# Kernel optimization log

Hardware: AMD Instinct MI355X
Metric: run time of the kernel (lower is better)

Reference implementation:

```python
import jax, jax.numpy as jnp
import numpy as np

EPS = 1e-5

def _bn(x, gamma, beta, mean, var):
    # eval-mode BatchNorm2d
    inv = gamma / jnp.sqrt(var + EPS)
    return x * inv[None, :, None, None] + (beta - mean * inv)[None, :, None, None]

def _conv(x, w):
    # Conv2d kernel 3x3, padding=(1,0), no bias; width already circularly padded
    return jax.lax.conv_general_dilated(x, w, (1, 1), [(1, 1), (0, 0)],
                                        dimension_numbers=('NCHW', 'OIHW', 'NCHW'))

def _circ_pad_w(x):
    # F.pad(x, (1,1,0,0), mode='circular')
    return jnp.pad(x, ((0, 0), (0, 0), (0, 0), (1, 1)), mode='wrap')

def _forward(flow_matrix, polar_fea, range_fea,
             fusion_w, fusion_gamma, fusion_beta, fusion_mean, fusion_var,
             attn_w, attn_gamma, attn_beta, attn_mean, attn_var):
    N, C, Hr, Wr = range_fea.shape
    _, _, H, W = polar_fea.shape
    _, h, w, K, _ = flow_matrix.shape
    # nearest-resize flow grid to (H, W) (identity when h==H, w==W)
    ri = jnp.arange(H) * h // H
    ci = jnp.arange(W) * w // W
    flow = flow_matrix[:, ri][:, :, ci]                       # [N,H,W,K,2]
    # torch.flip(dims=[-1]) then pad z=0: grid x=flow[...,1], y=flow[...,0], z=0.
    # Din=1 and z=0 with align_corners=False => iz=0 exactly -> pure 2D bilinear.
    gx = flow[..., 1]
    gy = flow[..., 0]
    ix = ((gx + 1.0) * Wr - 1.0) * 0.5                        # [N,H,W,K]
    iy = ((gy + 1.0) * Hr - 1.0) * 0.5
    feat_flat = range_fea.reshape(N, C, Hr * Wr)

    def gather(yi, xi):
        # yi, xi: [N,H,W] int32; zeros padding outside
        valid = (yi >= 0) & (yi < Hr) & (xi >= 0) & (xi < Wr)
        lin = jnp.clip(yi, 0, Hr - 1) * Wr + jnp.clip(xi, 0, Wr - 1)
        v = jax.vmap(lambda f, l: jnp.take(f, l.reshape(-1), axis=1))(feat_flat, lin)
        v = v.reshape(N, C, H, W)
        return v * valid[:, None].astype(v.dtype)

    def step(carry, grid_k):
        ixk, iyk = grid_k                                     # [N,H,W]
        x0 = jnp.floor(ixk); y0 = jnp.floor(iyk)
        wx1 = ixk - x0;      wy1 = iyk - y0
        x0i = x0.astype(jnp.int32); y0i = y0.astype(jnp.int32)
        val = (((1 - wy1) * (1 - wx1))[:, None] * gather(y0i,     x0i)
             + ((1 - wy1) * wx1)[:, None]       * gather(y0i,     x0i + 1)
             + (wy1 * (1 - wx1))[:, None]       * gather(y0i + 1, x0i)
             + (wy1 * wx1)[:, None]             * gather(y0i + 1, x0i + 1))
        return jnp.maximum(carry, val), None

    init = jnp.full((N, C, H, W), -jnp.inf, range_fea.dtype)
    grids = (jnp.moveaxis(ix, -1, 0), jnp.moveaxis(iy, -1, 0))  # [K,N,H,W]
    flow_fea, _ = jax.lax.scan(step, init, grids)               # max over K samples

    fea = jnp.concatenate([polar_fea, flow_fea], axis=1)        # [N,2C,H,W]
    res = _conv(_circ_pad_w(fea), fusion_w)
    res = jax.nn.relu(_bn(res, fusion_gamma, fusion_beta, fusion_mean, fusion_var))
    att = _conv(_circ_pad_w(res), attn_w)
    att = jax.nn.softmax(_bn(att, attn_gamma, attn_beta, attn_mean, attn_var), axis=1)
    return polar_fea + res * att


def setup_inputs() -> dict:
    key = jax.random.key(0)
    ks = jax.random.split(key, 6)
    N, C, H, W, K, Hr, Wr = 1, 64, 480, 360, 32, 64, 2048
    flow_matrix = jax.random.uniform(ks[0], (N, H, W, K, 2), jnp.float32, -1.0, 1.0)
    polar_fea = jax.random.normal(ks[1], (N, C, H, W), jnp.float32)
    range_fea = jax.random.normal(ks[2], (N, C, Hr, Wr), jnp.float32)
    fusion_w = jax.random.normal(ks[3], (C, 2 * C, 3, 3), jnp.float32) * 0.02
    attn_w = jax.random.normal(ks[4], (C, C, 3, 3), jnp.float32) * 0.02
    ones = jnp.ones((C,), jnp.float32)
    zeros = jnp.zeros((C,), jnp.float32)
    return {
        'flow_matrix': flow_matrix, 'polar_fea': polar_fea, 'range_fea': range_fea,
        'fusion_w': fusion_w, 'fusion_gamma': ones, 'fusion_beta': zeros,
        'fusion_mean': zeros, 'fusion_var': ones,
        'attn_w': attn_w, 'attn_gamma': ones, 'attn_beta': zeros,
        'attn_mean': zeros, 'attn_var': ones,
    }


def reference(flow_matrix, polar_fea, range_fea,
              fusion_w, fusion_gamma, fusion_beta, fusion_mean, fusion_var,
              attn_w, attn_gamma, attn_beta, attn_mean, attn_var):
    return _forward(flow_matrix, polar_fea, range_fea,
                    fusion_w, fusion_gamma, fusion_beta, fusion_mean, fusion_var,
                    attn_w, attn_gamma, attn_beta, attn_mean, attn_var)
```

## Files before the change

### kernel.cpp

```cpp
#include <hip/hip_runtime.h>
#include <math.h>

#define CCH 64
#define HH 480
#define WW 360
#define KK 32
#define HR 64
#define WR 2048
#define NPIX (HH*WW)
#define RFNPIX (HR*WR)
#define ZOFF 16777216u
#define NEGOFF 16777344u

typedef __attribute__((ext_vector_type(8))) short short8;
typedef __attribute__((ext_vector_type(4))) float f32x4;
typedef __attribute__((ext_vector_type(4))) int  int4_;

__device__ __forceinline__ ushort f2bf(float f) {
    uint u = __float_as_uint(f);
    return (ushort)((u + 0x7fffu + ((u >> 16) & 1u)) >> 16);
}

__global__ __launch_bounds__(256) void k_wprep(const float* __restrict__ fw,
                                               const float* __restrict__ aw,
                                               ushort* __restrict__ wA1,
                                               ushort* __restrict__ wA2) {
    int t = blockIdx.x * 256 + threadIdx.x;
    if (t < 73728) {
        int j = t & 7, ln = (t >> 3) & 63, Mf = (t >> 9) & 3, rem = t >> 11;
        int tap = rem % 9, c = rem / 9;
        int o = Mf * 16 + (ln & 15);
        int ci = c * 32 + ((ln >> 4) & 3) * 8 + j;
        wA1[t] = f2bf(fw[(o * 128 + ci) * 9 + tap]);
    } else if (t < 73728 + 36864) {
        int i = t - 73728;
        int j = i & 7, ln = (i >> 3) & 63, Mf = (i >> 9) & 3, rem = i >> 11;
        int tap = rem % 9, c = rem / 9;
        int o = Mf * 16 + (ln & 15);
        int ci = c * 32 + ((ln >> 4) & 3) * 8 + j;
        wA2[i] = f2bf(aw[(o * 64 + ci) * 9 + tap]);
    }
}

__global__ __launch_bounds__(256) void k_tr(const float* __restrict__ src,
                                            ushort* __restrict__ dst,
                                            int npix, int rowShorts) {
    __shared__ float lds[64][65];
    int t = threadIdx.x;
    int pix0 = blockIdx.x * 64;
    int lx = t & 63, ty = t >> 6;
    #pragma unroll
    for (int cc = 0; cc < 64; cc += 4) {
        int c = cc + ty;
        lds[c][lx] = src[(size_t)c * npix + pix0 + lx];
    }
    __syncthreads();
    int cp = t & 31, po = t >> 5;
    #pragma unroll
    for (int pl = po; pl < 64; pl += 8) {
        uint u = (uint)f2bf(lds[2 * cp][pl]) | ((uint)f2bf(lds[2 * cp + 1][pl]) << 16);
        *(uint*)(dst + (size_t)(pix0 + pl) * rowShorts + cp * 2) = u;
    }
}

__global__ void k_zero(uint* __restrict__ rft32) {
    int t = threadIdx.x;
    if (t < 32)       rft32[(ZOFF >> 2) + t] = 0;
    else if (t < 64)  rft32[(NEGOFF >> 2) + (t - 32)] = 0xFF7FFF7Fu;
}

__global__ __launch_bounds__(256) void k_sample(const float* __restrict__ flow,
                                                const char* __restrict__ rftb,
                                                ushort* __restrict__ xin,
                                                int sel, int mergePrev) {
    __shared__ __align__(16) uint pbuf[4][2][33][8];
    int tid = threadIdx.x;
    int ln = tid & 63;
    int wid = tid >> 6;
    int half = ln >> 5;
    int gwave = blockIdx.x * 4 + wid;

    int k = ln & 31;
    int pix = gwave * 2 + half;
    const float* fp = flow + (size_t)pix * 64 + 2 * k;
    float gy = __builtin_nontemporal_load(fp);
    float gx = __builtin_nontemporal_load(fp + 1);
    float ix = fmaf(gx, 1024.f, 1023.5f);
    float iy = fmaf(gy, 32.f, 31.5f);
    float xf = floorf(ix), yf = floorf(iy);
    float wx = ix - xf, wy = iy - yf;
    int x0 = (int)xf, y0 = (int)yf;
    bool xv0 = (unsigned)x0 < (unsigned)WR;
    bool xv1 = (unsigned)(x0 + 1) < (unsigned)WR;
    bool yv0 = (unsigned)y0 < (unsigned)HR;
    bool yv1 = (unsigned)(y0 + 1) < (unsigned)HR;
    int xc0 = x0 < 0 ? 0 : x0;
    int xc1 = x0 + 1 > WR - 1 ? WR - 1 : x0 + 1;
    int yc0 = y0 < 0 ? 0 : y0;
    int yc1 = y0 + 1 > HR - 1 ? HR - 1 : y0 + 1;
    uint o00 = (xv0 && yv0) ? (uint)(((yc0 << 11) + xc0) << 7) : ZOFF;
    uint o01 = (xv1 && yv0) ? (uint)(((yc0 << 11) + xc1) << 7) : ZOFF;
    uint o10 = (xv0 && yv1) ? (uint)(((yc1 << 11) + xc0) << 7) : ZOFF;
    uint o11 = (xv1 && yv1) ? (uint)(((yc1 << 11) + xc1) << 7) : ZOFF;
    float w00 = (1.f - wy) * (1.f - wx);
    float w01 = (1.f - wy) * wx;
    float w10 = wy * (1.f - wx);
    float w11 = wy * wx;

    bool isIn = ((yc0 >> 5) == sel);
    unsigned long long hm = half ? 0xFFFFFFFF00000000ull : 0x00000000FFFFFFFFull;
    unsigned long long lower = (1ull << ln) - 1ull;
    unsigned long long balIn = __ballot(isIn);
    int cntIn = __popcll(balIn & hm);
    int rankIn = __popcll(balIn & hm & lower);
    int rankOut = __popcll(~balIn & hm & lower);
    int pos = isIn ? rankIn : (cntIn + rankOut);
    *(int4_*)&pbuf[wid][half][pos][0] =
        (int4_){(int)o00, __float_as_int(w00), (int)o01, __float_as_int(w01)};
    *(int4_*)&pbuf[wid][half][pos][4] =
        (int4_){(int)o10, __float_as_int(w10), (int)o11, __float_as_int(w11)};
    if ((ln & 31) == 0) {
        *(int4_*)&pbuf[wid][half][32][0] =
            (int4_){(int)NEGOFF, __float_as_int(1.0f), (int)ZOFF, 0};
        *(int4_*)&pbuf[wid][half][32][4] = (int4_){(int)ZOFF, 0, (int)ZOFF, 0};
    }
    __syncthreads();

    uint laneByte = (uint)((ln & 31) * 4);
    const uint* pb = &pbuf[wid][half][0][0];
    float mLo = -3.0e38f, mHi = -3.0e38f;
    int cA = __builtin_amdgcn_readlane(cntIn, 0);
    int cB = __builtin_amdgcn_readlane(cntIn, 32);
    int trip = cA > cB ? cA : cB;

    for (int i = 0; i < trip; i++) {
        int idx = (i < cntIn) ? i : 32;
        const uint* e = pb + idx * 8;
        uint2 e0 = *(const uint2*)(e + 0);
        uint2 e1 = *(const uint2*)(e + 2);
        uint2 e2 = *(const uint2*)(e + 4);
        uint2 e3 = *(const uint2*)(e + 6);
        uint d0 = *(const uint*)(rftb + (e0.x + laneByte));
        uint d1 = *(const uint*)(rftb + (e1.x + laneByte));
        uint d2 = *(const uint*)(rftb + (e2.x + laneByte));
        uint d3 = *(const uint*)(rftb + (e3.x + laneByte));
        float W0 = __uint_as_float(e0.y);
        float W1 = __uint_as_float(e1.y);
        float W2 = __uint_as_float(e2.y);
        float W3 = __uint_as_float(e3.y);

        float vlo = W0 * __uint_as_float(d0 << 16);
        vlo = fmaf(W1, __uint_as_float(d1 << 16), vlo);
        vlo = fmaf(W2, __uint_as_float(d2 << 16), vlo);
        vlo = fmaf(W3, __uint_as_float(d3 << 16), vlo);
        float vhi = W0 * __uint_as_float(d0 & 0xffff0000u);
        vhi = fmaf(W1, __uint_as_float(d1 & 0xffff0000u), vhi);
        vhi = fmaf(W2, __uint_as_float(d2 & 0xffff0000u), vhi);
        vhi = fmaf(W3, __uint_as_float(d3 & 0xffff0000u), vhi);
        mLo = fmaxf(mLo, vlo);
        mHi = fmaxf(mHi, vhi);
    }

    uint* xp = (uint*)((char*)xin + (size_t)pix * 256 + 128 + (ln & 31) * 4);
    if (mergePrev) {
        uint cur = __builtin_nontemporal_load(xp);
        mLo = fmaxf(mLo, __uint_as_float(cur << 16));
        mHi = fmaxf(mHi, __uint_as_float(cur & 0xffff0000u));
    }
    uint outw;
    asm("v_cvt_pk_bf16_f32 %0, %1, %2" : "=v"(outw) : "v"(mLo), "v"(mHi));
    __builtin_nontemporal_store(outw, xp);
}

__global__ __launch_bounds__(256) void k_mconv1(const ushort* __restrict__ xin,
                                                const ushort* __restrict__ wA,
                                                const float* __restrict__ g,
                                                const float* __restrict__ b,
                                                const float* __restrict__ mn,
                                                const float* __restrict__ vr,
                                                ushort* __restrict__ res_bf) {
    __shared__ __align__(16) ushort xt[3][194][32];
    int tid = threadIdx.x;
    int h = blockIdx.x >> 1, w0 = (blockIdx.x & 1) * 180;
    int wid = tid >> 6, ln = tid & 63;
    f32x4 acc[4][3];
    #pragma unroll
    for (int m = 0; m < 4; m++)
        #pragma unroll
        for (int nf = 0; nf < 3; nf++) acc[m][nf] = (f32x4){0.f, 0.f, 0.f, 0.f};

    for (int c = 0; c < 4; c++) {
        __syncthreads();
        for (int i = tid; i < 2184; i += 256) {
            int q = i & 3, s = i >> 2;
            int r = s / 182, pw = s - r * 182;
            int gh = h + r - 1;
            int gw = w0 + pw - 1;
            if (gw < 0) gw += WW;
            if (gw >= WW) gw -= WW;
            int4_ val = {0, 0, 0, 0};
            if ((unsigned)gh < (unsigned)HH)
                val = *(const int4_*)(xin + ((size_t)(gh * WW + gw) * 128 + c * 32 + q * 8));
            *(int4_*)&xt[r][pw][(q ^ (pw & 3)) * 8] = val;
        }
        __syncthreads();
        #pragma unroll
        for (int tap = 0; tap < 9; tap++) {
            int dh = tap / 3, dw = tap % 3;
            short8 aF[4];
            #pragma unroll
            for (int m = 0; m < 4; m++)
                aF[m] = *(const short8*)(wA + (size_t)(((c * 9 + tap) * 4 + m) * 64 + ln) * 8);
            short8 bF[3];
            #pragma unroll
            for (int nf = 0; nf < 3; nf++) {
                int pw = wid * 48 + nf * 16 + (ln & 15) + dw;
                bF[nf] = *(const short8*)&xt[dh][pw][((((ln >> 4) & 3)) ^ (pw & 3)) * 8];
            }
            #pragma unroll
            for (int m = 0; m < 4; m++)
                #pragma unroll
                for (int nf = 0; nf < 3; nf++)
                    acc[m][nf] = __builtin_amdgcn_mfma_f32_16x16x32_bf16(aF[m], bF[nf], acc[m][nf], 0, 0, 0);
        }
    }
    #pragma unroll
    for (int m = 0; m < 4; m++) {
        int ob = m * 16 + ((ln >> 4) & 3) * 4;
        float sc0 = g[ob]     * rsqrtf(vr[ob]     + 1e-5f);
        float sc1 = g[ob + 1] * rsqrtf(vr[ob + 1] + 1e-5f);
        float sc2 = g[ob + 2] * rsqrtf(vr[ob + 2] + 1e-5f);
        float sc3 = g[ob + 3] * rsqrtf(vr[ob + 3] + 1e-5f);
        float bi0 = b[ob]     - mn[ob]     * sc0;
        float bi1 = b[ob + 1] - mn[ob + 1] * sc1;
        float bi2 = b[ob + 2] - mn[ob + 2] * sc2;
        float bi3 = b[ob + 3] - mn[ob + 3] * sc3;
        #pragma unroll
        for (int nf = 0; nf < 3; nf++) {
            int n = wid * 48 + nf * 16 + (ln & 15);
            if (n < 180) {
                int P = h * WW + w0 + n;
                float v0 = fmaxf(fmaf(acc[m][nf][0], sc0, bi0), 0.f);
                float v1 = fmaxf(fmaf(acc[m][nf][1], sc1, bi1), 0.f);
                float v2 = fmaxf(fmaf(acc[m][nf][2], sc2, bi2), 0.f);
                float v3 = fmaxf(fmaf(acc[m][nf][3], sc3, bi3), 0.f);
                uint lo, hi;
                asm("v_cvt_pk_bf16_f32 %0, %1, %2" : "=v"(lo) : "v"(v0), "v"(v1));
                asm("v_cvt_pk_bf16_f32 %0, %1, %2" : "=v"(hi) : "v"(v2), "v"(v3));
                uint2 pk; pk.x = lo; pk.y = hi;
                *(uint2*)(res_bf + (size_t)P * 64 + ob) = pk;
            }
        }
    }
}

__global__ __launch_bounds__(256) void k_mconv2(const ushort* __restrict__ res_bf,
                                                const float* __restrict__ polar,
                                                const ushort* __restrict__ wA,
                                                const float* __restrict__ g,
                                                const float* __restrict__ b,
                                                const float* __restrict__ mn,
                                                const float* __restrict__ vr,
                                                float* __restrict__ out) {
    __shared__ __align__(16) ushort xt[3][194][32];
    int tid = threadIdx.x;
    int h = blockIdx.x >> 1, w0 = (blockIdx.x & 1) * 180;
    int wid = tid >> 6, ln = tid & 63;
    f32x4 acc[4][3];
    #pragma unroll
    for (int m = 0; m < 4; m++)
        #pragma unroll
        for (int nf = 0; nf < 3; nf++) acc[m][nf] = (f32x4){0.f, 0.f, 0.f, 0.f};

    for (int c = 0; c < 2; c++) {
        __syncthreads();
        for (int i = tid; i < 2184; i += 256) {
            int q = i & 3, s = i >> 2;
            int r = s / 182, pw = s - r * 182;
            int gh = h + r - 1;
            int gw = w0 + pw - 1;
            if (gw < 0) gw += WW;
            if (gw >= WW) gw -= WW;
            int4_ val = {0, 0, 0, 0};
            if ((unsigned)gh < (unsigned)HH)
                val = *(const int4_*)(res_bf + ((size_t)(gh * WW + gw) * 64 + c * 32 + q * 8));
            *(int4_*)&xt[r][pw][(q ^ (pw & 3)) * 8] = val;
        }
        __syncthreads();
        #pragma unroll
        for (int tap = 0; tap < 9; tap++) {
            int dh = tap / 3, dw = tap % 3;
            short8 aF[4];
            #pragma unroll
            for (int m = 0; m < 4; m++)
                aF[m] = *(const short8*)(wA + (size_t)(((c * 9 + tap) * 4 + m) * 64 + ln) * 8);
            short8 bF[3];
            #pragma unroll
            for (int nf = 0; nf < 3; nf++) {
                int pw = wid * 48 + nf * 16 + (ln & 15) + dw;
                bF[nf] = *(const short8*)&xt[dh][pw][((((ln >> 4) & 3)) ^ (pw & 3)) * 8];
            }
            #pragma unroll
            for (int m = 0; m < 4; m++)
                #pragma unroll
                for (int nf = 0; nf < 3; nf++)
                    acc[m][nf] = __builtin_amdgcn_mfma_f32_16x16x32_bf16(aF[m], bF[nf], acc[m][nf], 0, 0, 0);
        }
    }
    #pragma unroll
    for (int m = 0; m < 4; m++) {
        #pragma unroll
        for (int reg = 0; reg < 4; reg++) {
            int o = m * 16 + ((ln >> 4) & 3) * 4 + reg;
            float sc = g[o] * rsqrtf(vr[o] + 1e-5f);
            float bi = b[o] - mn[o] * sc;
            #pragma unroll
            for (int nf = 0; nf < 3; nf++)
                acc[m][nf][reg] = fmaf(acc[m][nf][reg], sc, bi);
        }
    }
    #pragma unroll
    for (int nf = 0; nf < 3; nf++) {
        float mx = -3.0e38f;
        #pragma unroll
        for (int m = 0; m < 4; m++)
            #pragma unroll
            for (int reg = 0; reg < 4; reg++) mx = fmaxf(mx, acc[m][nf][reg]);
        mx = fmaxf(mx, __shfl_xor(mx, 16));
        mx = fmaxf(mx, __shfl_xor(mx, 32));
        float s = 0.f;
        #pragma unroll
        for (int m = 0; m < 4; m++)
            #pragma unroll
            for (int reg = 0; reg < 4; reg++) {
                float e = __expf(acc[m][nf][reg] - mx);
                acc[m][nf][reg] = e;
                s += e;
            }
        s += __shfl_xor(s, 16);
        s += __shfl_xor(s, 32);
        float rinv = 1.f / s;
        int n = wid * 48 + nf * 16 + (ln & 15);
        if (n < 180) {
            int P = h * WW + w0 + n;
            #pragma unroll
            for (int m = 0; m < 4; m++)
                #pragma unroll
                for (int reg = 0; reg < 4; reg++) {
                    int o = m * 16 + ((ln >> 4) & 3) * 4 + reg;
                    float att = acc[m][nf][reg] * rinv;
                    float rv = __uint_as_float((uint)res_bf[(size_t)P * 64 + o] << 16);
                    out[(size_t)o * NPIX + P] =
                        fmaf(rv, att, polar[(size_t)o * NPIX + P]);
                }
        }
    }
}

extern "C" void kernel_launch(void* const* d_in, const int* in_sizes, int n_in,
                              void* d_out, int out_size, void* d_ws, size_t ws_size,
                              hipStream_t stream) {
    const float* flow  = (const float*)d_in[0];
    const float* polar = (const float*)d_in[1];
    const float* rf    = (const float*)d_in[2];
    const float* fw    = (const float*)d_in[3];
    const float* fg    = (const float*)d_in[4];
    const float* fb    = (const float*)d_in[5];
    const float* fm    = (const float*)d_in[6];
    const float* fv    = (const float*)d_in[7];
    const float* aw    = (const float*)d_in[8];
    const float* ag    = (const float*)d_in[9];
    const float* ab    = (const float*)d_in[10];
    const float* am    = (const float*)d_in[11];
    const float* av    = (const float*)d_in[12];
    float* out = (float*)d_out;

    char* wsb = (char*)d_ws;
    ushort* xin    = (ushort*)wsb;
    ushort* rft    = (ushort*)(wsb + 44236800);
    ushort* res_bf = (ushort*)(wsb + 61014272);
    ushort* wA1    = (ushort*)(wsb + 83132672);
    ushort* wA2    = wA1 + 73728;

    k_wprep<<<432, 256, 0, stream>>>(fw, aw, wA1, wA2);
    k_tr<<<NPIX / 64, 256, 0, stream>>>(polar, xin, NPIX, 128);
    k_tr<<<RFNPIX / 64, 256, 0, stream>>>(rf, rft, RFNPIX, 64);
    k_zero<<<1, 64, 0, stream>>>((uint*)rft);
    k_sample<<<NPIX / 8, 256, 0, stream>>>(flow, (const char*)rft, xin, 0, 0);
    k_sample<<<NPIX / 8, 256, 0, stream>>>(flow, (const char*)rft, xin, 1, 1);
    k_mconv1<<<960, 256, 0, stream>>>(xin, wA1, fg, fb, fm, fv, res_bf);
    k_mconv2<<<960, 256, 0, stream>>>(res_bf, polar, wA2, ag, ab, am, av, out);
}
```

Measured before the change: 364.5 us.

## Load conv B-fragments directly from global memory instead of LDS staging

Both 3x3 conv MFMA kernels drop the shared-memory tile and its two barriers per channel chunk. Each lane now reads its bf16 input fragments straight from global memory using precomputed circular-wrapped column offsets, and skips rows that fall outside the image. This removes the LDS write/read round trip and the synchronisation, relying on L1/L2 to serve the neighbouring taps that reuse the same data. The cost is more global load instructions and exposed latency per MFMA group, with no LDS reuse across waves.

Measured after the change: 410.5 us. 12.6% more time.

```diff
diff --git a/kernel.cpp b/kernel.cpp
--- a/kernel.cpp
+++ b/kernel.cpp
@@ -179,54 +179,57 @@
                                                 const float* __restrict__ mn,
                                                 const float* __restrict__ vr,
                                                 ushort* __restrict__ res_bf) {
-    __shared__ __align__(16) ushort xt[3][194][32];
     int tid = threadIdx.x;
     int h = blockIdx.x >> 1, w0 = (blockIdx.x & 1) * 180;
     int wid = tid >> 6, ln = tid & 63;
-    f32x4 acc[4][3];
-    #pragma unroll
-    for (int m = 0; m < 4; m++)
-        #pragma unroll
-        for (int nf = 0; nf < 3; nf++) acc[m][nf] = (f32x4){0.f, 0.f, 0.f, 0.f};
-
-    for (int c = 0; c < 4; c++) {
-        __syncthreads();
-        for (int i = tid; i < 2184; i += 256) {
-            int q = i & 3, s = i >> 2;
-            int r = s / 182, pw = s - r * 182;
-            int gh = h + r - 1;
-            int gw = w0 + pw - 1;
+    int kq = (ln >> 4) & 3;
+    int nl = ln & 15;
+
+    int poff[3][3];
+    #pragma unroll
+    for (int dw = 0; dw < 3; dw++)
+        #pragma unroll
+        for (int nf = 0; nf < 3; nf++) {
+            int gw = w0 + wid * 48 + nf * 16 + nl + dw - 1;
             if (gw < 0) gw += WW;
             if (gw >= WW) gw -= WW;
-            int4_ val = {0, 0, 0, 0};
-            if ((unsigned)gh < (unsigned)HH)
-                val = *(const int4_*)(xin + ((size_t)(gh * WW + gw) * 128 + c * 32 + q * 8));
-            *(int4_*)&xt[r][pw][(q ^ (pw & 3)) * 8] = val;
-        }
-        __syncthreads();
-        #pragma unroll
-        for (int tap = 0; tap < 9; tap++) {
-            int dh = tap / 3, dw = tap % 3;
-            short8 aF[4];
-            #pragma unroll
-            for (int m = 0; m < 4; m++)
-                aF[m] = *(const short8*)(wA + (size_t)(((c * 9 + tap) * 4 + m) * 64 + ln) * 8);
-            short8 bF[3];
-            #pragma unroll
-            for (int nf = 0; nf < 3; nf++) {
-                int pw = wid * 48 + nf * 16 + (ln & 15) + dw;
-                bF[nf] = *(const short8*)&xt[dh][pw][((((ln >> 4) & 3)) ^ (pw & 3)) * 8];
+            poff[dw][nf] = gw * 128;
+        }
+
+    f32x4 acc[4][3];
+    #pragma unroll
+    for (int m = 0; m < 4; m++)
+        #pragma unroll
+        for (int nf = 0; nf < 3; nf++) acc[m][nf] = (f32x4){0.f, 0.f, 0.f, 0.f};
+
+    for (int c = 0; c < 4; c++) {
+        #pragma unroll
+        for (int dh = 0; dh < 3; dh++) {
+            int gh = h + dh - 1;
+            if ((unsigned)gh >= (unsigned)HH) continue;
+            const ushort* rowp = xin + (size_t)gh * (WW * 128) + c * 32 + kq * 8;
+            #pragma unroll
+            for (int dw = 0; dw < 3; dw++) {
+                int tap = dh * 3 + dw;
+                short8 aF[4];
+                #pragma unroll
+                for (int m = 0; m < 4; m++)
+                    aF[m] = *(const short8*)(wA + (size_t)(((c * 9 + tap) * 4 + m) * 64 + ln) * 8);
+                short8 bF[3];
+                #pragma unroll
+                for (int nf = 0; nf < 3; nf++)
+                    bF[nf] = *(const short8*)(rowp + poff[dw][nf]);
+                #pragma unroll
+                for (int m = 0; m < 4; m++)
+                    #pragma unroll
+                    for (int nf = 0; nf < 3; nf++)
+                        acc[m][nf] = __builtin_amdgcn_mfma_f32_16x16x32_bf16(aF[m], bF[nf], acc[m][nf], 0, 0, 0);
             }
-            #pragma unroll
-            for (int m = 0; m < 4; m++)
-                #pragma unroll
-                for (int nf = 0; nf < 3; nf++)
-                    acc[m][nf] = __builtin_amdgcn_mfma_f32_16x16x32_bf16(aF[m], bF[nf], acc[m][nf], 0, 0, 0);
         }
     }
     #pragma unroll
     for (int m = 0; m < 4; m++) {
-        int ob = m * 16 + ((ln >> 4) & 3) * 4;
+        int ob = m * 16 + kq * 4;
         float sc0 = g[ob]     * rsqrtf(vr[ob]     + 1e-5f);
         float sc1 = g[ob + 1] * rsqrtf(vr[ob + 1] + 1e-5f);
         float sc2 = g[ob + 2] * rsqrtf(vr[ob + 2] + 1e-5f);
@@ -237,7 +240,7 @@
         float bi3 = b[ob + 3] - mn[ob + 3] * sc3;
         #pragma unroll
         for (int nf = 0; nf < 3; nf++) {
-            int n = wid * 48 + nf * 16 + (ln & 15);
+            int n = wid * 48 + nf * 16 + nl;
             if (n < 180) {
                 int P = h * WW + w0 + n;
                 float v0 = fmaxf(fmaf(acc[m][nf][0], sc0, bi0), 0.f);
@@ -262,56 +265,59 @@
                                                 const float* __restrict__ mn,
                                                 const float* __restrict__ vr,
                                                 float* __restrict__ out) {
-    __shared__ __align__(16) ushort xt[3][194][32];
     int tid = threadIdx.x;
     int h = blockIdx.x >> 1, w0 = (blockIdx.x & 1) * 180;
     int wid = tid >> 6, ln = tid & 63;
-    f32x4 acc[4][3];
-    #pragma unroll
-    for (int m = 0; m < 4; m++)
-        #pragma unroll
-        for (int nf = 0; nf < 3; nf++) acc[m][nf] = (f32x4){0.f, 0.f, 0.f, 0.f};
-
-    for (int c = 0; c < 2; c++) {
-        __syncthreads();
-        for (int i = tid; i < 2184; i += 256) {
-            int q = i & 3, s = i >> 2;
-            int r = s / 182, pw = s - r * 182;
-            int gh = h + r - 1;
-            int gw = w0 + pw - 1;
+    int kq = (ln >> 4) & 3;
+    int nl = ln & 15;
+
+    int poff[3][3];
+    #pragma unroll
+    for (int dw = 0; dw < 3; dw++)
+        #pragma unroll
+        for (int nf = 0; nf < 3; nf++) {
+            int gw = w0 + wid * 48 + nf * 16 + nl + dw - 1;
             if (gw < 0) gw += WW;
             if (gw >= WW) gw -= WW;
-            int4_ val = {0, 0, 0, 0};
-            if ((unsigned)gh < (unsigned)HH)
-                val = *(const int4_*)(res_bf + ((size_t)(gh * WW + gw) * 64 + c * 32 + q * 8));
-            *(int4_*)&xt[r][pw][(q ^ (pw & 3)) * 8] = val;
-        }
-        __syncthreads();
-        #pragma unroll
-        for (int tap = 0; tap < 9; tap++) {
-            int dh = tap / 3, dw = tap % 3;
-            short8 aF[4];
-            #pragma unroll
-            for (int m = 0; m < 4; m++)
-                aF[m] = *(const short8*)(wA + (size_t)(((c * 9 + tap) * 4 + m) * 64 + ln) * 8);
-            short8 bF[3];
-            #pragma unroll
-            for (int nf = 0; nf < 3; nf++) {
-                int pw = wid * 48 + nf * 16 + (ln & 15) + dw;
-                bF[nf] = *(const short8*)&xt[dh][pw][((((ln >> 4) & 3)) ^ (pw & 3)) * 8];
+            poff[dw][nf] = gw * 64;
+        }
+
+    f32x4 acc[4][3];
+    #pragma unroll
+    for (int m = 0; m < 4; m++)
+        #pragma unroll
+        for (int nf = 0; nf < 3; nf++) acc[m][nf] = (f32x4){0.f, 0.f, 0.f, 0.f};
+
+    for (int c = 0; c < 2; c++) {
+        #pragma unroll
+        for (int dh = 0; dh < 3; dh++) {
+            int gh = h + dh - 1;
+            if ((unsigned)gh >= (unsigned)HH) continue;
+            const ushort* rowp = res_bf + (size_t)gh * (WW * 64) + c * 32 + kq * 8;
+            #pragma unroll
+            for (int dw = 0; dw < 3; dw++) {
+                int tap = dh * 3 + dw;
+                short8 aF[4];
+                #pragma unroll
+                for (int m = 0; m < 4; m++)
+                    aF[m] = *(const short8*)(wA + (size_t)(((c * 9 + tap) * 4 + m) * 64 + ln) * 8);
+                short8 bF[3];
+                #pragma unroll
+                for (int nf = 0; nf < 3; nf++)
+                    bF[nf] = *(const short8*)(rowp + poff[dw][nf]);
+                #pragma unroll
+                for (int m = 0; m < 4; m++)
+                    #pragma unroll
+                    for (int nf = 0; nf < 3; nf++)
+                        acc[m][nf] = __builtin_amdgcn_mfma_f32_16x16x32_bf16(aF[m], bF[nf], acc[m][nf], 0, 0, 0);
             }
-            #pragma unroll
-            for (int m = 0; m < 4; m++)
-                #pragma unroll
-                for (int nf = 0; nf < 3; nf++)
-                    acc[m][nf] = __builtin_amdgcn_mfma_f32_16x16x32_bf16(aF[m], bF[nf], acc[m][nf], 0, 0, 0);
         }
     }
     #pragma unroll
     for (int m = 0; m < 4; m++) {
         #pragma unroll
         for (int reg = 0; reg < 4; reg++) {
-            int o = m * 16 + ((ln >> 4) & 3) * 4 + reg;
+            int o = m * 16 + kq * 4 + reg;
             float sc = g[o] * rsqrtf(vr[o] + 1e-5f);
             float bi = b[o] - mn[o] * sc;
             #pragma unroll
@@ -340,14 +346,14 @@
         s += __shfl_xor(s, 16);
         s += __shfl_xor(s, 32);
         float rinv = 1.f / s;
-        int n = wid * 48 + nf * 16 + (ln & 15);
+        int n = wid * 48 + nf * 16 + nl;
         if (n < 180) {
             int P = h * WW + w0 + n;
             #pragma unroll
             for (int m = 0; m < 4; m++)
                 #pragma unroll
                 for (int reg = 0; reg < 4; reg++) {
-                    int o = m * 16 + ((ln >> 4) & 3) * 4 + reg;
+                    int o = m * 16 + kq * 4 + reg;
                     float att = acc[m][nf][reg] * rinv;
                     float rv = __uint_as_float((uint)res_bf[(size_t)P * 64 + o] << 16);
                     out[(size_t)o * NPIX + P] =
```
